# Optimization experiments

Hardware: AMD Instinct MI355X
Metric: run time of the kernel (lower is better)

The kernel has to match this reference:

```python
import jax, jax.numpy as jnp
import numpy as np

B, S, E, H = 2, 2048, 2048, 16
D = E // H  # head_dim = 128


def rotate_half(x):
    x1, x2 = jnp.split(x, 2, axis=-1)
    return jnp.concatenate([-x2, x1], axis=-1)


def rope_sincos(seq_len, dim):
    inv_freq = 1.0 / (10000.0 ** (jnp.arange(0, dim, 2, dtype=jnp.float32) / dim))
    t = jnp.arange(seq_len, dtype=jnp.float32)
    freqs = jnp.outer(t, inv_freq)            # [S, D/2]
    emb = jnp.concatenate([freqs, freqs], -1)  # [S, D]
    return jnp.sin(emb), jnp.cos(emb)


def apply_rope(x, sin, cos):
    # x: [B, S, H, D]; sin/cos: [S, D] -> [1, S, 1, D]
    sin = sin[None, :, None, :]
    cos = cos[None, :, None, :]
    return x * cos + rotate_half(x) * sin


def setup_inputs() -> dict:
    key = jax.random.key(0)
    k1, k2 = jax.random.split(key)
    x = jax.random.normal(k1, (B, S, E), dtype=jnp.float32)
    # causal boolean mask [B, 1, S, S]
    mask = jnp.broadcast_to(jnp.tril(jnp.ones((S, S), dtype=bool))[None, None], (B, 1, S, S))
    # fused QKV projection weight (hk.Linear, no bias): [E, 3E]
    W_qkv = jax.random.normal(k2, (E, 3 * E), dtype=jnp.float32) / np.sqrt(E)
    return {"x": x, "mask": mask, "W_qkv": W_qkv}


def reference(x, mask, W_qkv):
    seq_len = x.shape[1]
    qkv = x @ W_qkv                               # [B, S, 3E]
    q, k, v = jnp.split(qkv, 3, axis=-1)
    q = q.reshape(-1, seq_len, H, D)
    k = k.reshape(-1, seq_len, H, D)
    v = v.reshape(-1, seq_len, H, D)
    sin, cos = rope_sincos(seq_len, D)
    q = apply_rope(q, sin, cos)
    k = apply_rope(k, sin, cos)
    attn = jnp.einsum('bqhd,bkhd->bhqk', q, k) / jnp.sqrt(jnp.float32(D))
    m = jnp.broadcast_to(mask, (mask.shape[0], H, seq_len, k.shape[1]))
    attn = jnp.where(m, attn, -jnp.inf)
    attn = jax.nn.softmax(attn, axis=-1)
    out = jnp.einsum('bhqk,bkhd->bqhd', attn, v)
    return out.reshape(-1, seq_len, H * D)
```

## Files before the change

### kernel.cpp

```cpp
#include <hip/hip_runtime.h>

typedef __bf16 bf16;
typedef __bf16 bf16x8 __attribute__((ext_vector_type(8)));
typedef __bf16 bf16x4 __attribute__((ext_vector_type(4)));
typedef float f32x4 __attribute__((ext_vector_type(4)));

#define MFMA16(a, b, c) __builtin_amdgcn_mfma_f32_16x16x32_bf16(a, b, c, 0, 0, 0)

#define Bq 2
#define Sq 2048
#define Eq 2048
#define Hq 16
#define Dq 128
#define N3E 6144

#define GLOAD_LDS16(gp, lp) \
  __builtin_amdgcn_global_load_lds( \
      (const __attribute__((address_space(1))) void*)(gp), \
      (__attribute__((address_space(3))) void*)(lp), 16, 0, 0)

__device__ __forceinline__ bf16 f2bf(float f) {
  unsigned u = __builtin_bit_cast(unsigned, f);
  u += 0x7FFFu + ((u >> 16) & 1u);
  unsigned short h = (unsigned short)(u >> 16);
  return __builtin_bit_cast(bf16, h);
}
__device__ __forceinline__ float bf2f(bf16 b) {
  unsigned short h = __builtin_bit_cast(unsigned short, b);
  return __builtin_bit_cast(float, (unsigned)h << 16);
}

__global__ __launch_bounds__(256) void prep(const float* __restrict__ x,
                                            bf16* __restrict__ xb,
                                            const float* __restrict__ w,
                                            bf16* __restrict__ wt,
                                            float2* __restrict__ tbl) {
  __shared__ __align__(16) bf16 T[64][72];
  const int tid = threadIdx.x;
  const int bidx = blockIdx.x;

  if (bidx < 4096) {
    const size_t i = ((size_t)bidx * 256 + tid) * 8;
    float4 a = *(const float4*)(x + i);
    float4 b = *(const float4*)(x + i + 4);
    bf16x8 o;
    o[0] = f2bf(a.x); o[1] = f2bf(a.y); o[2] = f2bf(a.z); o[3] = f2bf(a.w);
    o[4] = f2bf(b.x); o[5] = f2bf(b.y); o[6] = f2bf(b.z); o[7] = f2bf(b.w);
    *(bf16x8*)(xb + i) = o;
  } else if (bidx < 4096 + 3072) {
    const int b2 = bidx - 4096;
    const int kb = b2 & 31;
    const int nb = b2 >> 5;
    const int k0 = kb * 64, n0 = nb * 64;
    {
      const int kr = tid >> 4, nc = (tid & 15) * 4;
#pragma unroll
      for (int p = 0; p < 4; ++p) {
        const int k = kr + p * 16;
        float4 v = *(const float4*)(w + (size_t)(k0 + k) * N3E + n0 + nc);
        T[nc + 0][k] = f2bf(v.x);
        T[nc + 1][k] = f2bf(v.y);
        T[nc + 2][k] = f2bf(v.z);
        T[nc + 3][k] = f2bf(v.w);
      }
    }
    __syncthreads();
#pragma unroll
    for (int q = 0; q < 2; ++q) {
      const int id = q * 256 + tid;
      const int n = id >> 3, ch = id & 7;
      bf16x8 v = *(const bf16x8*)&T[n][ch * 8];
      *(bf16x8*)(wt + (size_t)(n0 + n) * Eq + k0 + ch * 8) = v;
    }
  } else {
    const int i = (bidx - 7168) * 256 + tid;
    const int s = i >> 6, d = i & 63;
    const float freq = __expf(-(float)d * 0.14391157f);
    const float ang = (float)s * freq;
    float sv, cv;
    __sincosf(ang, &sv, &cv);
    tbl[i] = make_float2(cv, sv);
  }
}

__global__ __launch_bounds__(512, 2) void gemm_qkv(
    const bf16* __restrict__ xb, const bf16* __restrict__ wt,
    const float2* __restrict__ tbl, bf16* __restrict__ qws,
    bf16* __restrict__ kws, bf16* __restrict__ vtws) {
  __shared__ __align__(16) bf16 LDS[3 * 24576];

  const int tid = threadIdx.x;
  const int lane = tid & 63, wv = tid >> 6;
  const int q4 = lane >> 4, c = lane & 15;
  const int wm = (wv >> 2) * 64;
  const int wn = (wv & 3) * 64;
  const int cx = c & 7;

  const int bid = blockIdx.x;
  const int wg = (bid & 7) * 96 + (bid >> 3);
  const int m0 = (wg / 24) * 128;
  const int n0 = (wg % 24) * 256;

  f32x4 acc[4][4];
#pragma unroll
  for (int i = 0; i < 4; ++i)
#pragma unroll
    for (int j = 0; j < 4; ++j) acc[i][j] = {0.f, 0.f, 0.f, 0.f};

  const int NT = Eq / 64;

  auto stage = [&](int t, int st) {
    bf16* ab = LDS + st * 24576;
    bf16* bb = ab + 8192;
    const int k0 = t * 64;
#pragma unroll
    for (int it = 0; it < 2; ++it) {
      const int slot = it * 512 + tid;
      const int row = slot >> 3, kch = slot & 7;
      const int kcs = kch ^ (row & 7);
      GLOAD_LDS16(xb + (size_t)(m0 + row) * Eq + k0 + kcs * 8, ab + slot * 8);
    }
#pragma unroll
    for (int it = 0; it < 4; ++it) {
      const int slot = it * 512 + tid;
      const int row = slot >> 3, kch = slot & 7;
      const int kcs = kch ^ (row & 7);
      GLOAD_LDS16(wt + (size_t)(n0 + row) * Eq + k0 + kcs * 8, bb + slot * 8);
    }
  };

  stage(0, 0);
  stage(1, 1);
  asm volatile("s_waitcnt vmcnt(6)" ::: "memory");
  __builtin_amdgcn_s_barrier();

  int stC = 0;
#pragma unroll 1
  for (int t = 0; t < NT; ++t) {
    if (t + 2 < NT) {
      int ss = stC + 2;
      if (ss >= 3) ss -= 3;
      stage(t + 2, ss);
    }
    const bf16* A = LDS + stC * 24576;
    const bf16* Bb = A + 8192;
#pragma unroll
    for (int kk = 0; kk < 64; kk += 32) {
      const int bch = kk >> 3;
      bf16x8 af[4], bfr[4];
#pragma unroll
      for (int i = 0; i < 4; ++i)
        af[i] = *(const bf16x8*)
            &A[(wm + i * 16 + c) * 64 + ((bch + q4) ^ cx) * 8];
#pragma unroll
      for (int j = 0; j < 4; ++j)
        bfr[j] = *(const bf16x8*)
            &Bb[(wn + j * 16 + c) * 64 + ((bch + q4) ^ cx) * 8];
      __builtin_amdgcn_s_setprio(1);
#pragma unroll
      for (int i = 0; i < 4; ++i)
#pragma unroll
        for (int j = 0; j < 4; ++j)
          acc[i][j] = MFMA16(af[i], bfr[j], acc[i][j]);
      __builtin_amdgcn_s_setprio(0);
    }
    if (t + 1 < NT) {
      if (t + 2 < NT) asm volatile("s_waitcnt vmcnt(6)" ::: "memory");
      else            asm volatile("s_waitcnt vmcnt(0)" ::: "memory");
      __builtin_amdgcn_s_barrier();
    }
    stC = stC == 2 ? 0 : stC + 1;
  }
  __syncthreads();

  const int t3 = n0 >> 11;
  const int b = m0 >> 11;
  const int s0 = m0 & 2047;
  const int h0 = (n0 & 2047) >> 7;

  bf16* E = LDS;

  if (t3 == 2) {
#pragma unroll 1
    for (int hh = 0; hh < 2; ++hh) {
      if (((wv & 3) >> 1) == hh) {
#pragma unroll
        for (int i = 0; i < 4; ++i)
#pragma unroll
          for (int j = 0; j < 4; ++j) {
            bf16x4 pv;
            pv[0] = f2bf(acc[i][j][0]); pv[1] = f2bf(acc[i][j][1]);
            pv[2] = f2bf(acc[i][j][2]); pv[3] = f2bf(acc[i][j][3]);
            *(bf16x4*)&E[((wn & 127) + j * 16 + c) * 136 + wm + i * 16 +
                         q4 * 4] = pv;
          }
      }
      __syncthreads();
      bf16* vbase = vtws + ((size_t)(b * Hq + h0 + hh) * Dq) * Sq + s0;
#pragma unroll
      for (int p = 0; p < 4; ++p) {
        const int id = p * 512 + tid;
        const int d = id >> 4, ch = id & 15;
        bf16x8 v = *(const bf16x8*)&E[d * 136 + ch * 8];
        *(bf16x8*)&vbase[(size_t)d * Sq + ch * 8] = v;
      }
      __syncthreads();
    }
  } else {
#pragma unroll 1
    for (int hh = 0; hh < 2; ++hh) {
      if (((wv & 3) >> 1) == hh) {
#pragma unroll
        for (int i = 0; i < 4; ++i)
#pragma unroll
          for (int j = 0; j < 4; ++j)
#pragma unroll
            for (int rr = 0; rr < 4; ++rr)
              E[(wm + i * 16 + q4 * 4 + rr) * 136 + (wn & 127) + j * 16 + c] =
                  f2bf(acc[i][j][rr]);
      }
      __syncthreads();
      bf16* hd = ((t3 == 0) ? qws : kws) +
                 ((size_t)(b * Hq + h0 + hh) * Sq + s0) * Dq;
#pragma unroll
      for (int p = 0; p < 2; ++p) {
        const int row = p * 64 + (tid >> 3);
        const int dlow = (tid & 7) * 8;
        const int s = s0 + row;
        bf16x8 lo = *(const bf16x8*)&E[row * 136 + dlow];
        bf16x8 hi = *(const bf16x8*)&E[row * 136 + 64 + dlow];
        const float2* tb = tbl + (size_t)s * 64 + dlow;
        bf16x8 olo, ohi;
#pragma unroll
        for (int e = 0; e < 8; ++e) {
          const float cv = tb[e].x, sv = tb[e].y;
          const float x1 = bf2f(lo[e]), x2 = bf2f(hi[e]);
          olo[e] = f2bf(x1 * cv - x2 * sv);
          ohi[e] = f2bf(x2 * cv + x1 * sv);
        }
        *(bf16x8*)&hd[(size_t)row * Dq + dlow] = olo;
        *(bf16x8*)&hd[(size_t)row * Dq + 64 + dlow] = ohi;
      }
      __syncthreads();
    }
  }
}

#define KSC (0.08838834764831845f * 1.4426950408889634f)

__global__ __launch_bounds__(256, 2) void attn_kernel(
    const bf16* __restrict__ qws, const bf16* __restrict__ kws,
    const bf16* __restrict__ vtws, float* __restrict__ out,
    float* __restrict__ opart, float* __restrict__ ml) {
  __shared__ __align__(16) bf16 Kld[2][8192];
  __shared__ __align__(16) bf16 Vld[2][8192];
  __shared__ __align__(16) bf16 Plds[4][16][72];

  const int tid = threadIdx.x, lane = tid & 63, wave = tid >> 6;
  const int q4 = lane >> 4, c = lane & 15;
  const int h = blockIdx.y, b = blockIdx.z;

  const int xid = blockIdx.x;
  int qt, c0, c1, sp;
  bool split;
  if (xid < 16) {
    split = true;
    qt = 15 - (xid >> 1);
    sp = xid & 1;
    c0 = sp * (qt + 1);
    c1 = c0 + (qt + 1);
  } else {
    split = false;
    qt = 23 - xid;
    sp = 0;
    c0 = 0;
    c1 = 2 * qt + 2;
  }

  const size_t bh = (size_t)(b * Hq + h);
  const bf16* qbase = qws + bh * Sq * Dq;
  const bf16* kbase = kws + bh * Sq * Dq;
  const bf16* vbase = vtws + bh * Dq * Sq;
  const int q0 = qt * 128 + wave * 32;

  bf16x8 qf[2][4];
#pragma unroll
  for (int g = 0; g < 2; ++g)
#pragma unroll
    for (int ks = 0; ks < 4; ++ks)
      qf[g][ks] = *(const bf16x8*)
          &qbase[(size_t)(q0 + g * 16 + c) * Dq + ks * 32 + q4 * 8];

  f32x4 Ot[2][8];
  float m_i[2], l_i[2];
#pragma unroll
  for (int g = 0; g < 2; ++g) {
#pragma unroll
    for (int dj = 0; dj < 8; ++dj) Ot[g][dj] = {0.f, 0.f, 0.f, 0.f};
    m_i[g] = -1e30f; l_i[g] = 0.f;
  }

  {
    const int koff0 = c0 * 64;
#pragma unroll
    for (int it = 0; it < 4; ++it) {
      const int slot = it * 256 + tid;
      GLOAD_LDS16(kbase + (size_t)(koff0 + (slot & 63)) * Dq + (slot >> 6) * 8,
                  &Kld[c0 & 1][slot * 8]);
      GLOAD_LDS16(vbase + (size_t)(slot & 127) * Sq + koff0 + (slot >> 7) * 8,
                  &Vld[c0 & 1][slot * 8]);
    }
  }
  __syncthreads();

  for (int kb = c0; kb < c1; ++kb) {
    const int buf = kb & 1;
    if (kb + 1 < c1) {
      const int nb = buf ^ 1;
      const int koff = (kb + 1) * 64;
#pragma unroll
      for (int it = 0; it < 4; ++it) {
        const int slot = it * 256 + tid;
        GLOAD_LDS16(kbase + (size_t)(koff + (slot & 63)) * Dq + (slot >> 6) * 8,
                    &Kld[nb][slot * 8]);
        GLOAD_LDS16(vbase + (size_t)(slot & 127) * Sq + koff + (slot >> 7) * 8,
                    &Vld[nb][slot * 8]);
      }
    }
    const bool masked = (kb >= 2 * qt);
#pragma unroll
    for (int g = 0; g < 2; ++g) {
      const int qg = q0 + g * 16 + c;
      f32x4 st[4];
#pragma unroll
      for (int j8 = 0; j8 < 4; ++j8) st[j8] = {0.f, 0.f, 0.f, 0.f};
      __builtin_amdgcn_s_setprio(1);
#pragma unroll
      for (int ks = 0; ks < 4; ++ks) {
        const bf16x8 qv = qf[g][ks];
#pragma unroll
        for (int j8 = 0; j8 < 4; ++j8) {
          const bf16x8 kv = *(const bf16x8*)
              &Kld[buf][((ks * 4 + q4) * 64 + j8 * 16 + c) * 8];
          st[j8] = MFMA16(kv, qv, st[j8]);
        }
      }
      __builtin_amdgcn_s_setprio(0);
      if (masked) {
        const int kb64 = kb * 64 + q4 * 4;
#pragma unroll
        for (int j8 = 0; j8 < 4; ++j8)
#pragma unroll
          for (int rr = 0; rr < 4; ++rr)
            if (kb64 + j8 * 16 + rr > qg) st[j8][rr] = -1e30f;
      }
      float mloc = -1e30f;
#pragma unroll
      for (int j8 = 0; j8 < 4; ++j8)
#pragma unroll
        for (int rr = 0; rr < 4; ++rr) mloc = fmaxf(mloc, st[j8][rr]);
      mloc = fmaxf(mloc, __shfl_xor(mloc, 16, 64));
      mloc = fmaxf(mloc, __shfl_xor(mloc, 32, 64));
      float mn = m_i[g];
      if (__any(mloc > mn)) {
        mn = fmaxf(mn, mloc);
        const float alpha = exp2f((m_i[g] - mn) * KSC);
        m_i[g] = mn;
        l_i[g] *= alpha;
#pragma unroll
        for (int dj = 0; dj < 8; ++dj) Ot[g][dj] *= alpha;
      }
      float ssum = 0.f;
#pragma unroll
      for (int j8 = 0; j8 < 4; ++j8)
#pragma unroll
        for (int rr = 0; rr < 4; ++rr) {
          const float p = exp2f((st[j8][rr] - mn) * KSC);
          st[j8][rr] = p;
          ssum += p;
        }
      ssum += __shfl_xor(ssum, 16, 64);
      ssum += __shfl_xor(ssum, 32, 64);
      l_i[g] += ssum;
#pragma unroll
      for (int j8 = 0; j8 < 4; ++j8) {
        bf16x4 pk;
        pk[0] = f2bf(st[j8][0]); pk[1] = f2bf(st[j8][1]);
        pk[2] = f2bf(st[j8][2]); pk[3] = f2bf(st[j8][3]);
        *(bf16x4*)&Plds[wave][c][j8 * 16 + q4 * 4] = pk;
      }
      __builtin_amdgcn_s_setprio(1);
#pragma unroll
      for (int ks = 0; ks < 2; ++ks) {
        const bf16x8 pv = *(const bf16x8*)&Plds[wave][c][ks * 32 + q4 * 8];
#pragma unroll
        for (int dj = 0; dj < 8; ++dj) {
          const bf16x8 vv = *(const bf16x8*)
              &Vld[buf][((ks * 4 + q4) * 128 + dj * 16 + c) * 8];
          Ot[g][dj] = MFMA16(vv, pv, Ot[g][dj]);
        }
      }
      __builtin_amdgcn_s_setprio(0);
    }
    __syncthreads();
  }

  if (!split) {
#pragma unroll
    for (int g = 0; g < 2; ++g) {
      const float inv = 1.0f / l_i[g];
      float* orow = out + ((size_t)b * Sq + q0 + g * 16 + c) * Eq + h * Dq;
#pragma unroll
      for (int dj = 0; dj < 8; ++dj) {
        float4 o;
        o.x = Ot[g][dj][0] * inv; o.y = Ot[g][dj][1] * inv;
        o.z = Ot[g][dj][2] * inv; o.w = Ot[g][dj][3] * inv;
        *(float4*)&orow[dj * 16 + q4 * 4] = o;
      }
    }
  } else {
    const int tix = (((b * Hq + h) * 8) + (qt - 8)) * 2 + sp;
#pragma unroll
    for (int g = 0; g < 2; ++g) {
      const int wrow = wave * 32 + g * 16 + c;
      float* prow = opart + ((size_t)tix * 128 + wrow) * 128;
#pragma unroll
      for (int dj = 0; dj < 8; ++dj) {
        float4 o;
        o.x = Ot[g][dj][0]; o.y = Ot[g][dj][1];
        o.z = Ot[g][dj][2]; o.w = Ot[g][dj][3];
        *(float4*)&prow[dj * 16 + q4 * 4] = o;
      }
      if (q4 == 0) {
        ml[((size_t)tix * 128 + wrow) * 2 + 0] = m_i[g];
        ml[((size_t)tix * 128 + wrow) * 2 + 1] = l_i[g];
      }
    }
  }
}

__global__ __launch_bounds__(256) void attn_combine(
    const float* __restrict__ opart, const float* __restrict__ ml,
    float* __restrict__ out) {
  const int tile = blockIdx.x;
  const int qt = (tile & 7) + 8;
  const int hb = tile >> 3;
  const int h = hb & 15, b = hb >> 4;
  const int tid = threadIdx.x;
  const int r = tid >> 1;
  const int d0 = (tid & 1) * 64;
  const int t0 = tile * 2, t1 = t0 + 1;

  const float m0 = ml[((size_t)t0 * 128 + r) * 2 + 0];
  const float l0 = ml[((size_t)t0 * 128 + r) * 2 + 1];
  const float m1 = ml[((size_t)t1 * 128 + r) * 2 + 0];
  const float l1 = ml[((size_t)t1 * 128 + r) * 2 + 1];
  const float m = fmaxf(m0, m1);
  const float w0 = exp2f((m0 - m) * KSC);
  const float w1 = exp2f((m1 - m) * KSC);
  const float inv = 1.0f / (l0 * w0 + l1 * w1);
  const float s0 = w0 * inv, s1 = w1 * inv;

  const float* p0 = opart + ((size_t)t0 * 128 + r) * 128 + d0;
  const float* p1 = opart + ((size_t)t1 * 128 + r) * 128 + d0;
  float* orow = out + ((size_t)(b * Sq + qt * 128 + r)) * Eq + h * Dq + d0;
#pragma unroll
  for (int i = 0; i < 16; ++i) {
    float4 a = *(const float4*)&p0[i * 4];
    float4 bb = *(const float4*)&p1[i * 4];
    float4 o;
    o.x = a.x * s0 + bb.x * s1;
    o.y = a.y * s0 + bb.y * s1;
    o.z = a.z * s0 + bb.z * s1;
    o.w = a.w * s0 + bb.w * s1;
    *(float4*)&orow[i * 4] = o;
  }
}

extern "C" void kernel_launch(void* const* d_in, const int* in_sizes, int n_in,
                              void* d_out, int out_size, void* d_ws,
                              size_t ws_size, hipStream_t stream) {
  const float* x = (const float*)d_in[0];
  const float* w = (const float*)d_in[2];
  float* out = (float*)d_out;

  const size_t nX = (size_t)Bq * Sq * Eq;
  const size_t nW = (size_t)Eq * N3E;
  const size_t perT = (size_t)Bq * Hq * Sq * Dq;

  bf16* xb = (bf16*)d_ws;
  bf16* wt = xb + nX;
  bf16* qws = wt + nW;
  bf16* kws = qws + perT;
  bf16* vtws = kws + perT;
  float2* tbl = (float2*)(vtws + perT);

  float* opart = (float*)d_ws;
  float* ml = opart + (size_t)512 * 128 * 128;

  prep<<<7680, 256, 0, stream>>>(x, xb, w, wt, tbl);

  gemm_qkv<<<768, 512, 0, stream>>>(xb, wt, tbl, qws, kws, vtws);

  dim3 g3(24, 16, 2);
  attn_kernel<<<g3, 256, 0, stream>>>(qws, kws, vtws, out, opart, ml);

  attn_combine<<<256, 256, 0, stream>>>(opart, ml, out);
}
```

Before: 396.7 us.

## Pack attention work into 16 balanced blocks per head via lookup tables

Replaces the 24-blocks-per-head causal attention grid with 16 blocks per head. Each block processes one or two work segments (split halves or full query tiles) taken from constant lookup tables, so every block does a similar amount of work. A permutation for batch 1 staggers the ordering across the grid. The aim is to cut tail imbalance and the launch to 512 blocks so it fits in one wave across the CUs, at the cost of serialising two segments inside some blocks and reading the tables from device memory.

Result: faster. 371.3 us (-6.4%).

```diff
diff --git a/kernel.cpp b/kernel.cpp
--- a/kernel.cpp
+++ b/kernel.cpp
@@ -248,6 +248,12 @@
 
 #define KSC (0.08838834764831845f * 1.4426950408889634f)
 
+__device__ const int dSQT0[16] = {15,15, 7,14,14, 6,13,13,12,12,11,11, 8,10,10, 9};
+__device__ const int dSSP0[16] = { 0, 1, 2, 0, 1, 2, 0, 1, 0, 1, 0, 1, 0, 0, 1, 0};
+__device__ const int dSQT1[16] = {-1,-1,-1,-1,-1,-1,-1,-1, 0, 1, 2, 3, 5, 8, 4, 9};
+__device__ const int dSSP1[16] = { 0, 0, 0, 0, 0, 0, 0, 0, 2, 2, 2, 2, 2, 1, 2, 1};
+__device__ const int dZP[16]   = { 9, 2, 1,13,15,12,14,11,10, 0, 8, 7, 5, 3, 6, 4};
+
 __global__ __launch_bounds__(256, 2) void attn_kernel(
     const bf16* __restrict__ qws, const bf16* __restrict__ kws,
     const bf16* __restrict__ vtws, float* __restrict__ out,
@@ -259,181 +265,179 @@
   const int tid = threadIdx.x, lane = tid & 63, wave = tid >> 6;
   const int q4 = lane >> 4, c = lane & 15;
   const int h = blockIdx.y, b = blockIdx.z;
-
-  const int xid = blockIdx.x;
-  int qt, c0, c1, sp;
-  bool split;
-  if (xid < 16) {
-    split = true;
-    qt = 15 - (xid >> 1);
-    sp = xid & 1;
-    c0 = sp * (qt + 1);
-    c1 = c0 + (qt + 1);
-  } else {
-    split = false;
-    qt = 23 - xid;
-    sp = 0;
-    c0 = 0;
-    c1 = 2 * qt + 2;
-  }
+  const int sidx = (b == 0) ? blockIdx.x : dZP[blockIdx.x];
 
   const size_t bh = (size_t)(b * Hq + h);
   const bf16* qbase = qws + bh * Sq * Dq;
   const bf16* kbase = kws + bh * Sq * Dq;
   const bf16* vbase = vtws + bh * Dq * Sq;
-  const int q0 = qt * 128 + wave * 32;
-
-  bf16x8 qf[2][4];
-#pragma unroll
-  for (int g = 0; g < 2; ++g)
-#pragma unroll
-    for (int ks = 0; ks < 4; ++ks)
-      qf[g][ks] = *(const bf16x8*)
-          &qbase[(size_t)(q0 + g * 16 + c) * Dq + ks * 32 + q4 * 8];
-
-  f32x4 Ot[2][8];
-  float m_i[2], l_i[2];
-#pragma unroll
-  for (int g = 0; g < 2; ++g) {
-#pragma unroll
-    for (int dj = 0; dj < 8; ++dj) Ot[g][dj] = {0.f, 0.f, 0.f, 0.f};
-    m_i[g] = -1e30f; l_i[g] = 0.f;
-  }
-
-  {
-    const int koff0 = c0 * 64;
-#pragma unroll
-    for (int it = 0; it < 4; ++it) {
-      const int slot = it * 256 + tid;
-      GLOAD_LDS16(kbase + (size_t)(koff0 + (slot & 63)) * Dq + (slot >> 6) * 8,
-                  &Kld[c0 & 1][slot * 8]);
-      GLOAD_LDS16(vbase + (size_t)(slot & 127) * Sq + koff0 + (slot >> 7) * 8,
-                  &Vld[c0 & 1][slot * 8]);
-    }
-  }
-  __syncthreads();
-
-  for (int kb = c0; kb < c1; ++kb) {
-    const int buf = kb & 1;
-    if (kb + 1 < c1) {
-      const int nb = buf ^ 1;
-      const int koff = (kb + 1) * 64;
+
+#pragma unroll 1
+  for (int seg = 0; seg < 2; ++seg) {
+    const int qt = (seg == 0) ? dSQT0[sidx] : dSQT1[sidx];
+    if (qt < 0) break;
+    const int sp = (seg == 0) ? dSSP0[sidx] : dSSP1[sidx];
+    const bool split = (sp != 2);
+    const int c0 = split ? sp * (qt + 1) : 0;
+    const int c1 = split ? c0 + (qt + 1) : 2 * qt + 2;
+    const int q0 = qt * 128 + wave * 32;
+
+    bf16x8 qf[2][4];
+#pragma unroll
+    for (int g = 0; g < 2; ++g)
+#pragma unroll
+      for (int ks = 0; ks < 4; ++ks)
+        qf[g][ks] = *(const bf16x8*)
+            &qbase[(size_t)(q0 + g * 16 + c) * Dq + ks * 32 + q4 * 8];
+
+    f32x4 Ot[2][8];
+    float m_i[2], l_i[2];
+#pragma unroll
+    for (int g = 0; g < 2; ++g) {
+#pragma unroll
+      for (int dj = 0; dj < 8; ++dj) Ot[g][dj] = {0.f, 0.f, 0.f, 0.f};
+      m_i[g] = -1e30f; l_i[g] = 0.f;
+    }
+
+    {
+      const int koff0 = c0 * 64;
 #pragma unroll
       for (int it = 0; it < 4; ++it) {
         const int slot = it * 256 + tid;
-        GLOAD_LDS16(kbase + (size_t)(koff + (slot & 63)) * Dq + (slot >> 6) * 8,
-                    &Kld[nb][slot * 8]);
-        GLOAD_LDS16(vbase + (size_t)(slot & 127) * Sq + koff + (slot >> 7) * 8,
-                    &Vld[nb][slot * 8]);
-      }
-    }
-    const bool masked = (kb >= 2 * qt);
-#pragma unroll
-    for (int g = 0; g < 2; ++g) {
-      const int qg = q0 + g * 16 + c;
-      f32x4 st[4];
-#pragma unroll
-      for (int j8 = 0; j8 < 4; ++j8) st[j8] = {0.f, 0.f, 0.f, 0.f};
-      __builtin_amdgcn_s_setprio(1);
-#pragma unroll
-      for (int ks = 0; ks < 4; ++ks) {
-        const bf16x8 qv = qf[g][ks];
+        GLOAD_LDS16(
+            kbase + (size_t)(koff0 + (slot & 63)) * Dq + (slot >> 6) * 8,
+            &Kld[c0 & 1][slot * 8]);
+        GLOAD_LDS16(
+            vbase + (size_t)(slot & 127) * Sq + koff0 + (slot >> 7) * 8,
+            &Vld[c0 & 1][slot * 8]);
+      }
+    }
+    __syncthreads();
+
+    for (int kb = c0; kb < c1; ++kb) {
+      const int buf = kb & 1;
+      if (kb + 1 < c1) {
+        const int nb = buf ^ 1;
+        const int koff = (kb + 1) * 64;
+#pragma unroll
+        for (int it = 0; it < 4; ++it) {
+          const int slot = it * 256 + tid;
+          GLOAD_LDS16(
+              kbase + (size_t)(koff + (slot & 63)) * Dq + (slot >> 6) * 8,
+              &Kld[nb][slot * 8]);
+          GLOAD_LDS16(
+              vbase + (size_t)(slot & 127) * Sq + koff + (slot >> 7) * 8,
+              &Vld[nb][slot * 8]);
+        }
+      }
+      const bool masked = (kb >= 2 * qt);
+#pragma unroll
+      for (int g = 0; g < 2; ++g) {
+        const int qg = q0 + g * 16 + c;
+        f32x4 st[4];
+#pragma unroll
+        for (int j8 = 0; j8 < 4; ++j8) st[j8] = {0.f, 0.f, 0.f, 0.f};
+        __builtin_amdgcn_s_setprio(1);
+#pragma unroll
+        for (int ks = 0; ks < 4; ++ks) {
+          const bf16x8 qv = qf[g][ks];
+#pragma unroll
+          for (int j8 = 0; j8 < 4; ++j8) {
+            const bf16x8 kv = *(const bf16x8*)
+                &Kld[buf][((ks * 4 + q4) * 64 + j8 * 16 + c) * 8];
+            st[j8] = MFMA16(kv, qv, st[j8]);
+          }
+        }
+        __builtin_amdgcn_s_setprio(0);
+        if (masked) {
+          const int kb64 = kb * 64 + q4 * 4;
+#pragma unroll
+          for (int j8 = 0; j8 < 4; ++j8)
+#pragma unroll
+            for (int rr = 0; rr < 4; ++rr)
+              if (kb64 + j8 * 16 + rr > qg) st[j8][rr] = -1e30f;
+        }
+        float mloc = -1e30f;
+#pragma unroll
+        for (int j8 = 0; j8 < 4; ++j8)
+#pragma unroll
+          for (int rr = 0; rr < 4; ++rr) mloc = fmaxf(mloc, st[j8][rr]);
+        mloc = fmaxf(mloc, __shfl_xor(mloc, 16, 64));
+        mloc = fmaxf(mloc, __shfl_xor(mloc, 32, 64));
+        float mn = m_i[g];
+        if (__any(mloc > mn)) {
+          mn = fmaxf(mn, mloc);
+          const float alpha = exp2f((m_i[g] - mn) * KSC);
+          m_i[g] = mn;
+          l_i[g] *= alpha;
+#pragma unroll
+          for (int dj = 0; dj < 8; ++dj) Ot[g][dj] *= alpha;
+        }
+        float ssum = 0.f;
+#pragma unroll
+        for (int j8 = 0; j8 < 4; ++j8)
+#pragma unroll
+          for (int rr = 0; rr < 4; ++rr) {
+            const float p = exp2f((st[j8][rr] - mn) * KSC);
+            st[j8][rr] = p;
+            ssum += p;
+          }
+        ssum += __shfl_xor(ssum, 16, 64);
+        ssum += __shfl_xor(ssum, 32, 64);
+        l_i[g] += ssum;
 #pragma unroll
         for (int j8 = 0; j8 < 4; ++j8) {
-          const bf16x8 kv = *(const bf16x8*)
-              &Kld[buf][((ks * 4 + q4) * 64 + j8 * 16 + c) * 8];
-          st[j8] = MFMA16(kv, qv, st[j8]);
-        }
-      }
-      __builtin_amdgcn_s_setprio(0);
-      if (masked) {
-        const int kb64 = kb * 64 + q4 * 4;
-#pragma unroll
-        for (int j8 = 0; j8 < 4; ++j8)
-#pragma unroll
-          for (int rr = 0; rr < 4; ++rr)
-            if (kb64 + j8 * 16 + rr > qg) st[j8][rr] = -1e30f;
-      }
-      float mloc = -1e30f;
-#pragma unroll
-      for (int j8 = 0; j8 < 4; ++j8)
-#pragma unroll
-        for (int rr = 0; rr < 4; ++rr) mloc = fmaxf(mloc, st[j8][rr]);
-      mloc = fmaxf(mloc, __shfl_xor(mloc, 16, 64));
-      mloc = fmaxf(mloc, __shfl_xor(mloc, 32, 64));
-      float mn = m_i[g];
-      if (__any(mloc > mn)) {
-        mn = fmaxf(mn, mloc);
-        const float alpha = exp2f((m_i[g] - mn) * KSC);
-        m_i[g] = mn;
-        l_i[g] *= alpha;
-#pragma unroll
-        for (int dj = 0; dj < 8; ++dj) Ot[g][dj] *= alpha;
-      }
-      float ssum = 0.f;
-#pragma unroll
-      for (int j8 = 0; j8 < 4; ++j8)
-#pragma unroll
-        for (int rr = 0; rr < 4; ++rr) {
-          const float p = exp2f((st[j8][rr] - mn) * KSC);
-          st[j8][rr] = p;
-          ssum += p;
-        }
-      ssum += __shfl_xor(ssum, 16, 64);
-      ssum += __shfl_xor(ssum, 32, 64);
-      l_i[g] += ssum;
-#pragma unroll
-      for (int j8 = 0; j8 < 4; ++j8) {
-        bf16x4 pk;
-        pk[0] = f2bf(st[j8][0]); pk[1] = f2bf(st[j8][1]);
-        pk[2] = f2bf(st[j8][2]); pk[3] = f2bf(st[j8][3]);
-        *(bf16x4*)&Plds[wave][c][j8 * 16 + q4 * 4] = pk;
-      }
-      __builtin_amdgcn_s_setprio(1);
-#pragma unroll
-      for (int ks = 0; ks < 2; ++ks) {
-        const bf16x8 pv = *(const bf16x8*)&Plds[wave][c][ks * 32 + q4 * 8];
+          bf16x4 pk;
+          pk[0] = f2bf(st[j8][0]); pk[1] = f2bf(st[j8][1]);
+          pk[2] = f2bf(st[j8][2]); pk[3] = f2bf(st[j8][3]);
+          *(bf16x4*)&Plds[wave][c][j8 * 16 + q4 * 4] = pk;
+        }
+        __builtin_amdgcn_s_setprio(1);
+#pragma unroll
+        for (int ks = 0; ks < 2; ++ks) {
+          const bf16x8 pv = *(const bf16x8*)&Plds[wave][c][ks * 32 + q4 * 8];
+#pragma unroll
+          for (int dj = 0; dj < 8; ++dj) {
+            const bf16x8 vv = *(const bf16x8*)
+                &Vld[buf][((ks * 4 + q4) * 128 + dj * 16 + c) * 8];
+            Ot[g][dj] = MFMA16(vv, pv, Ot[g][dj]);
+          }
+        }
+        __builtin_amdgcn_s_setprio(0);
+      }
+      __syncthreads();
+    }
+
+    if (!split) {
+#pragma unroll
+      for (int g = 0; g < 2; ++g) {
+        const float inv = 1.0f / l_i[g];
+        float* orow = out + ((size_t)b * Sq + q0 + g * 16 + c) * Eq + h * Dq;
 #pragma unroll
         for (int dj = 0; dj < 8; ++dj) {
-          const bf16x8 vv = *(const bf16x8*)
-              &Vld[buf][((ks * 4 + q4) * 128 + dj * 16 + c) * 8];
-          Ot[g][dj] = MFMA16(vv, pv, Ot[g][dj]);
-        }
-      }
-      __builtin_amdgcn_s_setprio(0);
-    }
-    __syncthreads();
-  }
-
-  if (!split) {
-#pragma unroll
-    for (int g = 0; g < 2; ++g) {
-      const float inv = 1.0f / l_i[g];
-      float* orow = out + ((size_t)b * Sq + q0 + g * 16 + c) * Eq + h * Dq;
-#pragma unroll
-      for (int dj = 0; dj < 8; ++dj) {
-        float4 o;
-        o.x = Ot[g][dj][0] * inv; o.y = Ot[g][dj][1] * inv;
-        o.z = Ot[g][dj][2] * inv; o.w = Ot[g][dj][3] * inv;
-        *(float4*)&orow[dj * 16 + q4 * 4] = o;
-      }
-    }
-  } else {
-    const int tix = (((b * Hq + h) * 8) + (qt - 8)) * 2 + sp;
-#pragma unroll
-    for (int g = 0; g < 2; ++g) {
-      const int wrow = wave * 32 + g * 16 + c;
-      float* prow = opart + ((size_t)tix * 128 + wrow) * 128;
-#pragma unroll
-      for (int dj = 0; dj < 8; ++dj) {
-        float4 o;
-        o.x = Ot[g][dj][0]; o.y = Ot[g][dj][1];
-        o.z = Ot[g][dj][2]; o.w = Ot[g][dj][3];
-        *(float4*)&prow[dj * 16 + q4 * 4] = o;
-      }
-      if (q4 == 0) {
-        ml[((size_t)tix * 128 + wrow) * 2 + 0] = m_i[g];
-        ml[((size_t)tix * 128 + wrow) * 2 + 1] = l_i[g];
+          float4 o;
+          o.x = Ot[g][dj][0] * inv; o.y = Ot[g][dj][1] * inv;
+          o.z = Ot[g][dj][2] * inv; o.w = Ot[g][dj][3] * inv;
+          *(float4*)&orow[dj * 16 + q4 * 4] = o;
+        }
+      }
+    } else {
+      const int tix = (((b * Hq + h) * 8) + (qt - 8)) * 2 + sp;
+#pragma unroll
+      for (int g = 0; g < 2; ++g) {
+        const int wrow = wave * 32 + g * 16 + c;
+        float* prow = opart + ((size_t)tix * 128 + wrow) * 128;
+#pragma unroll
+        for (int dj = 0; dj < 8; ++dj) {
+          float4 o;
+          o.x = Ot[g][dj][0]; o.y = Ot[g][dj][1];
+          o.z = Ot[g][dj][2]; o.w = Ot[g][dj][3];
+          *(float4*)&prow[dj * 16 + q4 * 4] = o;
+        }
+        if (q4 == 0) {
+          ml[((size_t)tix * 128 + wrow) * 2 + 0] = m_i[g];
+          ml[((size_t)tix * 128 + wrow) * 2 + 1] = l_i[g];
+        }
       }
     }
   }
@@ -502,7 +506,7 @@
 
   gemm_qkv<<<768, 512, 0, stream>>>(xb, wt, tbl, qws, kws, vtws);
 
-  dim3 g3(24, 16, 2);
+  dim3 g3(16, 16, 2);
   attn_kernel<<<g3, 256, 0, stream>>>(qws, kws, vtws, out, opart, ml);
 
   attn_combine<<<256, 256, 0, stream>>>(opart, ml, out);
```
